# Kernel optimization log

Hardware: AMD Instinct MI355X
Metric: run time of the kernel (lower is better)

## Reference

```python
import jax, jax.numpy as jnp
import numpy as np

B, T, J, D = 64, 2048, 128, 512


def setup_inputs() -> dict:
    key = jax.random.key(0)
    k1, k2, k3, k4 = jax.random.split(key, 4)
    question = jax.random.normal(k1, (B, J, D), dtype=jnp.float32)
    context = jax.random.normal(k2, (B, T, D), dtype=jnp.float32)
    question_len = jax.random.randint(k3, (B,), 1, J + 1, dtype=jnp.int32)
    context_len = jax.random.randint(k4, (B,), 1, T + 1, dtype=jnp.int32)
    weight = jnp.ones((D, 1), dtype=jnp.float32)  # initializer='ones'
    return {"question": question, "context": context,
            "question_len": question_len, "context_len": context_len,
            "weight": weight}


def reference(question, context, question_len, context_len, weight):
    # Original computes sum_d context[b,t,d]*question[b,j,d]*w[d] via a
    # broadcast [B,T,J,D] intermediate; reformulated as a batched GEMM.
    w = weight[:, 0]                                   # [D]
    sim = jnp.einsum('btd,bjd->btj', context * w, question)  # [B,T,J]
    Jm = question.shape[1]
    Tm = context.shape[1]
    q_mask = (jnp.arange(Jm) < question_len[:, None]).astype(jnp.float32)  # [B,J]
    c_mask = (jnp.arange(Tm) < context_len[:, None]).astype(jnp.float32)   # [B,T]
    mask = c_mask[:, :, None] * q_mask[:, None, :]     # [B,T,J]
    neg = jnp.finfo(jnp.float32).min
    sim = sim + neg * (1.0 - mask)
    attn = jax.nn.softmax(sim, axis=1)                 # softmax over context axis T
    return jnp.sum(attn * mask, axis=2)[..., None]     # [B,T,1]
```

## Files before the change

kernel.cpp:

```cpp
#include <hip/hip_runtime.h>
#include <stdint.h>
#include <math.h>

#define BB 64
#define TT 2048
#define JJ 128
#define DD 512
#define BK 32

typedef short short8 __attribute__((ext_vector_type(8)));
typedef float f32x4 __attribute__((ext_vector_type(4)));

__device__ inline unsigned pk_hi(float a, float b) {
  return __builtin_amdgcn_perm(__float_as_uint(b), __float_as_uint(a), 0x07060302u);
}
__device__ inline float truncbf(float x) {
  return __uint_as_float(__float_as_uint(x) & 0xFFFF0000u);
}
__device__ inline void pack8(float4 a, float4 b, uint4& h, uint4& l) {
  h = make_uint4(pk_hi(a.x, a.y), pk_hi(a.z, a.w), pk_hi(b.x, b.y), pk_hi(b.z, b.w));
  float l0 = a.x - truncbf(a.x), l1 = a.y - truncbf(a.y);
  float l2 = a.z - truncbf(a.z), l3 = a.w - truncbf(a.w);
  float l4 = b.x - truncbf(b.x), l5 = b.y - truncbf(b.y);
  float l6 = b.z - truncbf(b.z), l7 = b.w - truncbf(b.w);
  l = make_uint4(pk_hi(l0, l1), pk_hi(l2, l3), pk_hi(l4, l5), pk_hi(l6, l7));
}
__device__ inline short8 bc8(uint4 u) { return __builtin_bit_cast(short8, u); }

__global__ __launch_bounds__(256, 2)
void sim_gemm_mfma(const float* __restrict__ Qm, const float* __restrict__ w,
                   const float* __restrict__ Cm, const int* __restrict__ qlen,
                   const int* __restrict__ clen, float* __restrict__ S) {
  const int id = blockIdx.x;
  const int nid = (id & 7) * 128 + (id >> 3);
  const int b = nid >> 4;
  const int t0 = (nid & 15) * 128;

  const int cl = clen[b];
  if (t0 >= cl) return;
  const int ql = qlen[b];

  const int tid = threadIdx.x;
  const int lane = tid & 63;
  const int wv = tid >> 6;
  const int wm = (wv & 1) * 64;
  const int wn = (wv >> 1) * 64;
  const int l15 = lane & 15;
  const int q = lane >> 4;

  bool mact[4];
#pragma unroll
  for (int i = 0; i < 4; i++) mact[i] = (wm + i * 16) < ql;
  if (!mact[0]) return;

  const float* qa[4];
#pragma unroll
  for (int mi = 0; mi < 4; mi++)
    qa[mi] = Qm + ((size_t)b * JJ + wm + mi * 16 + l15) * DD + q * 8;
  const float* ca[4];
#pragma unroll
  for (int ni = 0; ni < 4; ni++)
    ca[ni] = Cm + ((size_t)b * TT + t0 + wn + ni * 16 + l15) * DD + q * 8;
  const float* wp = w + q * 8;

  f32x4 acc[4][4] = {};

  float4 pb0[4], pb1[4];
#pragma unroll
  for (int ni = 0; ni < 4; ni++) {
    pb0[ni] = *(const float4*)(ca[ni]);
    pb1[ni] = *(const float4*)(ca[ni] + 4);
  }

#pragma unroll 1
  for (int ks = 0; ks < 16; ks++) {
    float4 cv0[4], cv1[4];
#pragma unroll
    for (int ni = 0; ni < 4; ni++) { cv0[ni] = pb0[ni]; cv1[ni] = pb1[ni]; }
    if (ks < 15) {
#pragma unroll
      for (int ni = 0; ni < 4; ni++) {
        pb0[ni] = *(const float4*)(ca[ni] + (ks + 1) * BK);
        pb1[ni] = *(const float4*)(ca[ni] + (ks + 1) * BK + 4);
      }
    }
    const float4 w0 = *(const float4*)(wp + ks * BK);
    const float4 w1 = *(const float4*)(wp + ks * BK + 4);
    short8 ah[4], al[4];
#pragma unroll
    for (int mi = 0; mi < 4; mi++) {
      if (!mact[mi]) continue;
      float4 a0 = *(const float4*)(qa[mi] + ks * BK);
      float4 a1 = *(const float4*)(qa[mi] + ks * BK + 4);
      a0.x *= w0.x; a0.y *= w0.y; a0.z *= w0.z; a0.w *= w0.w;
      a1.x *= w1.x; a1.y *= w1.y; a1.z *= w1.z; a1.w *= w1.w;
      uint4 h, l;
      pack8(a0, a1, h, l);
      ah[mi] = bc8(h);
      al[mi] = bc8(l);
    }
    short8 bh[4], bl[4];
#pragma unroll
    for (int ni = 0; ni < 4; ni++) {
      uint4 h, l;
      pack8(cv0[ni], cv1[ni], h, l);
      bh[ni] = bc8(h);
      bl[ni] = bc8(l);
    }
#pragma unroll
    for (int mi = 0; mi < 4; mi++) {
      if (!mact[mi]) continue;
#pragma unroll
      for (int ni = 0; ni < 4; ni++) {
        acc[mi][ni] = __builtin_amdgcn_mfma_f32_16x16x32_bf16(ah[mi], bh[ni], acc[mi][ni], 0, 0, 0);
        acc[mi][ni] = __builtin_amdgcn_mfma_f32_16x16x32_bf16(al[mi], bh[ni], acc[mi][ni], 0, 0, 0);
        acc[mi][ni] = __builtin_amdgcn_mfma_f32_16x16x32_bf16(ah[mi], bl[ni], acc[mi][ni], 0, 0, 0);
      }
    }
  }

#pragma unroll
  for (int mi = 0; mi < 4; mi++) {
    if (!mact[mi]) continue;
#pragma unroll
    for (int ni = 0; ni < 4; ni++) {
      const int j = wm + mi * 16 + q * 4;
      const int t = t0 + wn + ni * 16 + l15;
      float* dst = S + ((size_t)b * JJ + j) * TT + t;
      dst[0 * TT] = acc[mi][ni][0];
      dst[1 * TT] = acc[mi][ni][1];
      dst[2 * TT] = acc[mi][ni][2];
      dst[3 * TT] = acc[mi][ni][3];
    }
  }
}

__global__ __launch_bounds__(256)
void softmax_stats_kernel(const float* __restrict__ S, const int* __restrict__ qlen,
                          const int* __restrict__ clen, float* __restrict__ m_out,
                          float* __restrict__ r_out) {
  const int j = blockIdx.x;
  const int b = blockIdx.y;
  if (j >= qlen[b]) return;
  const int cl = clen[b];
  const int tid = threadIdx.x;
  const float4* row = (const float4*)(S + ((size_t)b * JJ + j) * TT);

  const float NEG = -3.4e38f;
  float4 v0 = make_float4(NEG, NEG, NEG, NEG);
  float4 v1 = make_float4(NEG, NEG, NEG, NEG);
  const int t0 = tid * 4;
  const int t1 = (tid + 256) * 4;
  if (t0 < cl) v0 = row[tid];
  if (t1 < cl) v1 = row[tid + 256];

  float m = NEG;
  m = fmaxf(m, (t0 + 0 < cl) ? v0.x : NEG);
  m = fmaxf(m, (t0 + 1 < cl) ? v0.y : NEG);
  m = fmaxf(m, (t0 + 2 < cl) ? v0.z : NEG);
  m = fmaxf(m, (t0 + 3 < cl) ? v0.w : NEG);
  m = fmaxf(m, (t1 + 0 < cl) ? v1.x : NEG);
  m = fmaxf(m, (t1 + 1 < cl) ? v1.y : NEG);
  m = fmaxf(m, (t1 + 2 < cl) ? v1.z : NEG);
  m = fmaxf(m, (t1 + 3 < cl) ? v1.w : NEG);

  __shared__ float red[8];
#pragma unroll
  for (int off = 32; off > 0; off >>= 1) m = fmaxf(m, __shfl_down(m, off));
  if ((tid & 63) == 0) red[tid >> 6] = m;
  __syncthreads();
  m = fmaxf(fmaxf(red[0], red[1]), fmaxf(red[2], red[3]));

  float s = 0.f;
  s += (t0 + 0 < cl) ? __expf(v0.x - m) : 0.f;
  s += (t0 + 1 < cl) ? __expf(v0.y - m) : 0.f;
  s += (t0 + 2 < cl) ? __expf(v0.z - m) : 0.f;
  s += (t0 + 3 < cl) ? __expf(v0.w - m) : 0.f;
  s += (t1 + 0 < cl) ? __expf(v1.x - m) : 0.f;
  s += (t1 + 1 < cl) ? __expf(v1.y - m) : 0.f;
  s += (t1 + 2 < cl) ? __expf(v1.z - m) : 0.f;
  s += (t1 + 3 < cl) ? __expf(v1.w - m) : 0.f;
#pragma unroll
  for (int off = 32; off > 0; off >>= 1) s += __shfl_down(s, off);
  if ((tid & 63) == 0) red[4 + (tid >> 6)] = s;
  __syncthreads();
  s = red[4] + red[5] + red[6] + red[7];

  if (tid == 0) {
    m_out[(size_t)b * JJ + j] = m;
    r_out[(size_t)b * JJ + j] = 1.f / s;
  }
}

__global__ __launch_bounds__(256)
void out_kernel(const float* __restrict__ S, const float* __restrict__ m_arr,
                const float* __restrict__ r_arr, const int* __restrict__ qlen,
                const int* __restrict__ clen, float* __restrict__ out) {
  const int b = blockIdx.y;
  const int t = blockIdx.x * 256 + threadIdx.x;
  const int ql = qlen[b];
  const int cl = clen[b];

  __shared__ float lm[JJ];
  __shared__ float lr[JJ];
  if (threadIdx.x < ql) {
    lm[threadIdx.x] = m_arr[(size_t)b * JJ + threadIdx.x];
    lr[threadIdx.x] = r_arr[(size_t)b * JJ + threadIdx.x];
  }
  __syncthreads();

  float acc = 0.f;
  if (t < cl) {
    const float* col = S + (size_t)b * JJ * TT + t;
#pragma unroll 4
    for (int j = 0; j < ql; j++) {
      acc += __expf(col[(size_t)j * TT] - lm[j]) * lr[j];
    }
  }
  out[(size_t)b * TT + t] = acc;
}

extern "C" void kernel_launch(void* const* d_in, const int* in_sizes, int n_in,
                              void* d_out, int out_size, void* d_ws, size_t ws_size,
                              hipStream_t stream) {
  const float* question = (const float*)d_in[0];
  const float* context  = (const float*)d_in[1];
  const int*   qlen     = (const int*)d_in[2];
  const int*   clen     = (const int*)d_in[3];
  const float* weight   = (const float*)d_in[4];
  float* out = (float*)d_out;

  float* S = (float*)d_ws;
  float* m_arr = S + (size_t)BB * JJ * TT;
  float* r_arr = m_arr + (size_t)BB * JJ;

  sim_gemm_mfma<<<dim3(1024), 256, 0, stream>>>(question, weight, context, qlen, clen, S);
  softmax_stats_kernel<<<dim3(JJ, BB), 256, 0, stream>>>(S, qlen, clen, m_arr, r_arr);
  out_kernel<<<dim3(TT / 256, BB), 256, 0, stream>>>(S, m_arr, r_arr, qlen, clen, out);
}
```

Measured before the change: 432.1 us.

## Fuse GEMM, softmax stats and output reduction into one kernel with atomics

Replaces the three-kernel pipeline (similarity GEMM to workspace, per-row softmax stats, column sum) with a single kernel. Each block owns a 16-row question stripe across the full context length of one batch, so every block holds its entire score row in registers. It computes the row max and sum in-block and accumulates normalized contributions into the output with atomicAdd after a memset. This removes the round trip of the large B×J×T score matrix through global memory. In exchange, each block now keeps 32 accumulator tiles in registers, the grid shrinks to 512 blocks, and context data is reread once per stripe, which may lower occupancy and add load traffic.

```diff
diff --git a/kernel.cpp b/kernel.cpp
--- a/kernel.cpp
+++ b/kernel.cpp
@@ -28,196 +28,142 @@
 __device__ inline short8 bc8(uint4 u) { return __builtin_bit_cast(short8, u); }
 
 __global__ __launch_bounds__(256, 2)
-void sim_gemm_mfma(const float* __restrict__ Qm, const float* __restrict__ w,
-                   const float* __restrict__ Cm, const int* __restrict__ qlen,
-                   const int* __restrict__ clen, float* __restrict__ S) {
+void fused_attn(const float* __restrict__ Qm, const float* __restrict__ w,
+                const float* __restrict__ Cm, const int* __restrict__ qlen,
+                const int* __restrict__ clen, float* __restrict__ out) {
   const int id = blockIdx.x;
-  const int nid = (id & 7) * 128 + (id >> 3);
-  const int b = nid >> 4;
-  const int t0 = (nid & 15) * 128;
+  const int nid = (id & 7) * 64 + (id >> 3);
+  const int b = nid >> 3;
+  const int stripe = nid & 7;
 
+  const int ql = qlen[b];
+  if (stripe * 16 >= ql) return;
   const int cl = clen[b];
-  if (t0 >= cl) return;
-  const int ql = qlen[b];
 
   const int tid = threadIdx.x;
   const int lane = tid & 63;
   const int wv = tid >> 6;
-  const int wm = (wv & 1) * 64;
-  const int wn = (wv >> 1) * 64;
   const int l15 = lane & 15;
   const int q = lane >> 4;
+  const int t0w = wv * 512;
+  const int clw = cl - t0w;
 
-  bool mact[4];
+  const float* qa = Qm + ((size_t)b * JJ + stripe * 16 + l15) * DD + q * 8;
+  const float* wp = w + q * 8;
+  const float* cb[4];
 #pragma unroll
-  for (int i = 0; i < 4; i++) mact[i] = (wm + i * 16) < ql;
-  if (!mact[0]) return;
+  for (int i = 0; i < 4; i++)
+    cb[i] = Cm + ((size_t)b * TT + t0w + i * 16 + l15) * DD + q * 8;
 
-  const float* qa[4];
-#pragma unroll
-  for (int mi = 0; mi < 4; mi++)
-    qa[mi] = Qm + ((size_t)b * JJ + wm + mi * 16 + l15) * DD + q * 8;
-  const float* ca[4];
-#pragma unroll
-  for (int ni = 0; ni < 4; ni++)
-    ca[ni] = Cm + ((size_t)b * TT + t0 + wn + ni * 16 + l15) * DD + q * 8;
-  const float* wp = w + q * 8;
-
-  f32x4 acc[4][4] = {};
-
-  float4 pb0[4], pb1[4];
-#pragma unroll
-  for (int ni = 0; ni < 4; ni++) {
-    pb0[ni] = *(const float4*)(ca[ni]);
-    pb1[ni] = *(const float4*)(ca[ni] + 4);
-  }
+  f32x4 acc[32] = {};
 
 #pragma unroll 1
   for (int ks = 0; ks < 16; ks++) {
-    float4 cv0[4], cv1[4];
-#pragma unroll
-    for (int ni = 0; ni < 4; ni++) { cv0[ni] = pb0[ni]; cv1[ni] = pb1[ni]; }
-    if (ks < 15) {
-#pragma unroll
-      for (int ni = 0; ni < 4; ni++) {
-        pb0[ni] = *(const float4*)(ca[ni] + (ks + 1) * BK);
-        pb1[ni] = *(const float4*)(ca[ni] + (ks + 1) * BK + 4);
-      }
-    }
     const float4 w0 = *(const float4*)(wp + ks * BK);
     const float4 w1 = *(const float4*)(wp + ks * BK + 4);
-    short8 ah[4], al[4];
+    float4 a0 = *(const float4*)(qa + ks * BK);
+    float4 a1 = *(const float4*)(qa + ks * BK + 4);
+    a0.x *= w0.x; a0.y *= w0.y; a0.z *= w0.z; a0.w *= w0.w;
+    a1.x *= w1.x; a1.y *= w1.y; a1.z *= w1.z; a1.w *= w1.w;
+    uint4 h, l;
+    pack8(a0, a1, h, l);
+    const short8 ah = bc8(h);
+    const short8 al = bc8(l);
+
 #pragma unroll
-    for (int mi = 0; mi < 4; mi++) {
-      if (!mact[mi]) continue;
-      float4 a0 = *(const float4*)(qa[mi] + ks * BK);
-      float4 a1 = *(const float4*)(qa[mi] + ks * BK + 4);
-      a0.x *= w0.x; a0.y *= w0.y; a0.z *= w0.z; a0.w *= w0.w;
-      a1.x *= w1.x; a1.y *= w1.y; a1.z *= w1.z; a1.w *= w1.w;
-      uint4 h, l;
-      pack8(a0, a1, h, l);
-      ah[mi] = bc8(h);
-      al[mi] = bc8(l);
-    }
-    short8 bh[4], bl[4];
+    for (int g = 0; g < 8; g++) {
+      if (g * 64 < clw) {
+        float4 u0[4], u1[4];
 #pragma unroll
-    for (int ni = 0; ni < 4; ni++) {
-      uint4 h, l;
-      pack8(cv0[ni], cv1[ni], h, l);
-      bh[ni] = bc8(h);
-      bl[ni] = bc8(l);
-    }
+        for (int i = 0; i < 4; i++) {
+          const float* p = cb[i] + (size_t)g * (64 * DD) + ks * BK;
+          u0[i] = *(const float4*)p;
+          u1[i] = *(const float4*)(p + 4);
+        }
 #pragma unroll
-    for (int mi = 0; mi < 4; mi++) {
-      if (!mact[mi]) continue;
-#pragma unroll
-      for (int ni = 0; ni < 4; ni++) {
-        acc[mi][ni] = __builtin_amdgcn_mfma_f32_16x16x32_bf16(ah[mi], bh[ni], acc[mi][ni], 0, 0, 0);
-        acc[mi][ni] = __builtin_amdgcn_mfma_f32_16x16x32_bf16(al[mi], bh[ni], acc[mi][ni], 0, 0, 0);
-        acc[mi][ni] = __builtin_amdgcn_mfma_f32_16x16x32_bf16(ah[mi], bl[ni], acc[mi][ni], 0, 0, 0);
+        for (int i = 0; i < 4; i++) {
+          uint4 bhh, bll;
+          pack8(u0[i], u1[i], bhh, bll);
+          const short8 bh = bc8(bhh);
+          const short8 bl = bc8(bll);
+          acc[g * 4 + i] = __builtin_amdgcn_mfma_f32_16x16x32_bf16(ah, bh, acc[g * 4 + i], 0, 0, 0);
+          acc[g * 4 + i] = __builtin_amdgcn_mfma_f32_16x16x32_bf16(al, bh, acc[g * 4 + i], 0, 0, 0);
+          acc[g * 4 + i] = __builtin_amdgcn_mfma_f32_16x16x32_bf16(ah, bl, acc[g * 4 + i], 0, 0, 0);
+        }
       }
     }
   }
 
+  const float NEG = -3.4e38f;
+  __shared__ float mred[4][16];
+  __shared__ float sred[4][16];
+
+  float mr[4] = {NEG, NEG, NEG, NEG};
 #pragma unroll
-  for (int mi = 0; mi < 4; mi++) {
-    if (!mact[mi]) continue;
+  for (int nt = 0; nt < 32; nt++) {
+    const int t = t0w + nt * 16 + l15;
+    const bool v = t < cl;
 #pragma unroll
-    for (int ni = 0; ni < 4; ni++) {
-      const int j = wm + mi * 16 + q * 4;
-      const int t = t0 + wn + ni * 16 + l15;
-      float* dst = S + ((size_t)b * JJ + j) * TT + t;
-      dst[0 * TT] = acc[mi][ni][0];
-      dst[1 * TT] = acc[mi][ni][1];
-      dst[2 * TT] = acc[mi][ni][2];
-      dst[3 * TT] = acc[mi][ni][3];
+    for (int r = 0; r < 4; r++) mr[r] = fmaxf(mr[r], v ? acc[nt][r] : NEG);
+  }
+#pragma unroll
+  for (int off = 1; off < 16; off <<= 1) {
+#pragma unroll
+    for (int r = 0; r < 4; r++) mr[r] = fmaxf(mr[r], __shfl_xor(mr[r], off));
+  }
+  if (l15 == 0) {
+#pragma unroll
+    for (int r = 0; r < 4; r++) mred[wv][q * 4 + r] = mr[r];
+  }
+  __syncthreads();
+#pragma unroll
+  for (int r = 0; r < 4; r++) {
+    mr[r] = fmaxf(fmaxf(mred[0][q * 4 + r], mred[1][q * 4 + r]),
+                  fmaxf(mred[2][q * 4 + r], mred[3][q * 4 + r]));
+  }
+
+  float sr[4] = {0.f, 0.f, 0.f, 0.f};
+#pragma unroll
+  for (int nt = 0; nt < 32; nt++) {
+    const int t = t0w + nt * 16 + l15;
+    const bool v = t < cl;
+#pragma unroll
+    for (int r = 0; r < 4; r++) {
+      const float e = v ? __expf(acc[nt][r] - mr[r]) : 0.f;
+      acc[nt][r] = e;
+      sr[r] += e;
     }
   }
-}
-
-__global__ __launch_bounds__(256)
-void softmax_stats_kernel(const float* __restrict__ S, const int* __restrict__ qlen,
-                          const int* __restrict__ clen, float* __restrict__ m_out,
-                          float* __restrict__ r_out) {
-  const int j = blockIdx.x;
-  const int b = blockIdx.y;
-  if (j >= qlen[b]) return;
-  const int cl = clen[b];
-  const int tid = threadIdx.x;
-  const float4* row = (const float4*)(S + ((size_t)b * JJ + j) * TT);
-
-  const float NEG = -3.4e38f;
-  float4 v0 = make_float4(NEG, NEG, NEG, NEG);
-  float4 v1 = make_float4(NEG, NEG, NEG, NEG);
-  const int t0 = tid * 4;
-  const int t1 = (tid + 256) * 4;
-  if (t0 < cl) v0 = row[tid];
-  if (t1 < cl) v1 = row[tid + 256];
-
-  float m = NEG;
-  m = fmaxf(m, (t0 + 0 < cl) ? v0.x : NEG);
-  m = fmaxf(m, (t0 + 1 < cl) ? v0.y : NEG);
-  m = fmaxf(m, (t0 + 2 < cl) ? v0.z : NEG);
-  m = fmaxf(m, (t0 + 3 < cl) ? v0.w : NEG);
-  m = fmaxf(m, (t1 + 0 < cl) ? v1.x : NEG);
-  m = fmaxf(m, (t1 + 1 < cl) ? v1.y : NEG);
-  m = fmaxf(m, (t1 + 2 < cl) ? v1.z : NEG);
-  m = fmaxf(m, (t1 + 3 < cl) ? v1.w : NEG);
-
-  __shared__ float red[8];
 #pragma unroll
-  for (int off = 32; off > 0; off >>= 1) m = fmaxf(m, __shfl_down(m, off));
-  if ((tid & 63) == 0) red[tid >> 6] = m;
-  __syncthreads();
-  m = fmaxf(fmaxf(red[0], red[1]), fmaxf(red[2], red[3]));
-
-  float s = 0.f;
-  s += (t0 + 0 < cl) ? __expf(v0.x - m) : 0.f;
-  s += (t0 + 1 < cl) ? __expf(v0.y - m) : 0.f;
-  s += (t0 + 2 < cl) ? __expf(v0.z - m) : 0.f;
-  s += (t0 + 3 < cl) ? __expf(v0.w - m) : 0.f;
-  s += (t1 + 0 < cl) ? __expf(v1.x - m) : 0.f;
-  s += (t1 + 1 < cl) ? __expf(v1.y - m) : 0.f;
-  s += (t1 + 2 < cl) ? __expf(v1.z - m) : 0.f;
-  s += (t1 + 3 < cl) ? __expf(v1.w - m) : 0.f;
+  for (int off = 1; off < 16; off <<= 1) {
 #pragma unroll
-  for (int off = 32; off > 0; off >>= 1) s += __shfl_down(s, off);
-  if ((tid & 63) == 0) red[4 + (tid >> 6)] = s;
-  __syncthreads();
-  s = red[4] + red[5] + red[6] + red[7];
-
-  if (tid == 0) {
-    m_out[(size_t)b * JJ + j] = m;
-    r_out[(size_t)b * JJ + j] = 1.f / s;
+    for (int r = 0; r < 4; r++) sr[r] += __shfl_xor(sr[r], off);
   }
-}
-
-__global__ __launch_bounds__(256)
-void out_kernel(const float* __restrict__ S, const float* __restrict__ m_arr,
-                const float* __restrict__ r_arr, const int* __restrict__ qlen,
-                const int* __restrict__ clen, float* __restrict__ out) {
-  const int b = blockIdx.y;
-  const int t = blockIdx.x * 256 + threadIdx.x;
-  const int ql = qlen[b];
-  const int cl = clen[b];
-
-  __shared__ float lm[JJ];
-  __shared__ float lr[JJ];
-  if (threadIdx.x < ql) {
-    lm[threadIdx.x] = m_arr[(size_t)b * JJ + threadIdx.x];
-    lr[threadIdx.x] = r_arr[(size_t)b * JJ + threadIdx.x];
+  if (l15 == 0) {
+#pragma unroll
+    for (int r = 0; r < 4; r++) sred[wv][q * 4 + r] = sr[r];
   }
   __syncthreads();
+  float rr[4];
+#pragma unroll
+  for (int r = 0; r < 4; r++) {
+    const float s = sred[0][q * 4 + r] + sred[1][q * 4 + r] +
+                    sred[2][q * 4 + r] + sred[3][q * 4 + r];
+    rr[r] = 1.f / s;
+    if (stripe * 16 + q * 4 + r >= ql) rr[r] = 0.f;
+  }
 
-  float acc = 0.f;
-  if (t < cl) {
-    const float* col = S + (size_t)b * JJ * TT + t;
-#pragma unroll 4
-    for (int j = 0; j < ql; j++) {
-      acc += __expf(col[(size_t)j * TT] - lm[j]) * lr[j];
+  float* ob = out + (size_t)b * TT + t0w;
+#pragma unroll
+  for (int nt = 0; nt < 32; nt++) {
+    if (nt * 16 < clw) {
+      float c = acc[nt][0] * rr[0] + acc[nt][1] * rr[1] +
+                acc[nt][2] * rr[2] + acc[nt][3] * rr[3];
+      c += __shfl_xor(c, 16);
+      c += __shfl_xor(c, 32);
+      if (q == 0) atomicAdd(ob + nt * 16 + l15, c);
     }
   }
-  out[(size_t)b * TT + t] = acc;
 }
 
 extern "C" void kernel_launch(void* const* d_in, const int* in_sizes, int n_in,
@@ -230,11 +176,7 @@
   const float* weight   = (const float*)d_in[4];
   float* out = (float*)d_out;
 
-  float* S = (float*)d_ws;
-  float* m_arr = S + (size_t)BB * JJ * TT;
-  float* r_arr = m_arr + (size_t)BB * JJ;
-
-  sim_gemm_mfma<<<dim3(1024), 256, 0, stream>>>(question, weight, context, qlen, clen, S);
-  softmax_stats_kernel<<<dim3(JJ, BB), 256, 0, stream>>>(S, qlen, clen, m_arr, r_arr);
-  out_kernel<<<dim3(TT / 256, BB), 256, 0, stream>>>(S, m_arr, r_arr, qlen, clen, out);
+  hipMemsetAsync(out, 0, (size_t)BB * TT * sizeof(float), stream);
+  fused_attn<<<dim3(BB * 8), 256, 0, stream>>>(question, weight, context,
+                                               qlen, clen, out);
 }
```

New measurement: 509.2 us. +17.8%, slower.
